# Optimization experiments

Measured on AMD Instinct MI355X. Metric: run time of the kernel, lower is better.

The kernel has to match this reference:

```python
import jax, jax.numpy as jnp
import numpy as np

DIM = 1      # homological dimension
CARD = 50    # number of diagram points
H, W = 28, 28
D = 2        # len(Ip.shape)


def _cubical(X, dim=DIM, card=CARD):
    """Pure-numpy cubical persistence (gudhi semantics: lower-dim cells get the
    min of incident top-dimensional cells; finite pairs of dimension `dim`,
    positive persistence, sorted by persistence descending; returns flat
    (i,j) pixel indices of birth/death critical top cells, zero-padded to
    2*D*card int32 values). Mirrors the Cubical numpy_function in the repo."""
    X = np.asarray(X, dtype=np.float64)
    Hh, Ww = X.shape
    A, Bc = 2 * Hh - 1, 2 * Ww - 1
    n = A * Bc
    F = np.empty(n)                 # filtration value per cell
    P = np.empty(n, np.int64)       # flat pixel index of the top cell realizing F
    dms = np.empty(n, np.int64)     # cell dimension

    def cands(a, lim):
        if a % 2 == 1:
            return [(a - 1) // 2]
        return [r for r in (a // 2 - 1, a // 2) if 0 <= r < lim]

    for a in range(A):
        ris = cands(a, Hh)
        for b in range(Bc):
            cjs = cands(b, Ww)
            best = None
            bp = 0
            for r in ris:
                for c in cjs:
                    v = X[r, c]
                    if best is None or v < best:
                        best = v
                        bp = r * Ww + c
            idx = a * Bc + b
            F[idx] = best
            P[idx] = bp
            dms[idx] = (a & 1) + (b & 1)

    order = np.lexsort((np.arange(n), dms, F))   # sort by (F, dim, index)
    pos = np.empty(n, np.int64)
    pos[order] = np.arange(n)

    def faces(cell):
        a, b = divmod(cell, Bc)
        fs = []
        if a & 1:
            fs += [(a - 1) * Bc + b, (a + 1) * Bc + b]
        if b & 1:
            fs += [a * Bc + b - 1, a * Bc + b + 1]
        return fs

    # standard Z/2 boundary-matrix reduction
    Rcols = {}
    low_to_col = {}
    pairs = []
    for j in range(n):
        cell = order[j]
        col = set(int(pos[f]) for f in faces(cell))
        while col:
            l = max(col)
            k = low_to_col.get(l)
            if k is None:
                break
            col ^= Rcols[k]
        if col:
            l = max(col)
            low_to_col[l] = j
            Rcols[j] = col
            pairs.append((l, j))

    rows, pers = [], []
    for (i, j) in pairs:
        bc, dc = order[i], order[j]
        if dms[bc] != dim:
            continue
        pr = F[dc] - F[bc]
        if pr <= 0:
            continue
        rows.append((int(P[bc]), int(P[dc])))
        pers.append(pr)
    if rows:
        srt = np.argsort(np.asarray(pers))[::-1]   # persistence descending
        rows = [rows[k] for k in srt]

    inds = []
    for k in range(min(card, len(rows))):
        bi, di = rows[k]
        inds += [bi // Ww, bi % Ww, di // Ww, di % Ww]
    inds += [0] * (2 * D * card - len(inds))
    return np.asarray(inds, dtype=np.int32)


def setup_inputs() -> dict:
    key = jax.random.key(0)
    k1, k2 = jax.random.split(key)
    I = jax.random.normal(k1, (H, W, 2), dtype=jnp.float32)
    p = jax.random.normal(k2, (2, 1), dtype=jnp.float32)
    return {"I": I, "p": p}


def reference(I, p):
    # Ip = reshape(tensordot(I, p, 1), [28, 28])
    Ip = jnp.reshape(jnp.tensordot(I, p, 1), (H, W))
    inds = jax.pure_callback(
        lambda x: _cubical(np.asarray(x)),
        jax.ShapeDtypeStruct((2 * D * CARD,), jnp.int32),
        Ip,
    )
    inds = jax.lax.stop_gradient(inds).reshape(-1, D)   # [2*card, 2]
    # gather_nd(Ip, inds) then reshape to [card, 2]
    dgm = Ip[inds[:, 0], inds[:, 1]].reshape(-1, 2)
    return dgm
```

## Files before the change

### kernel.cpp

```cpp
#include <hip/hip_runtime.h>

#define IMG_H 28
#define IMG_W 28
#define AA 55
#define NCELL 3025
#define NEDGE 1512
#define NSQ 729
#define CARD 50
#define NW 24
#define CAP 160
#define BS 1024

typedef unsigned long long u64;
typedef unsigned int u32;
typedef unsigned short u16;

#define OFF_KEYSE   0
#define OFF_KEYSS   16384
#define OFF_IP      24576
#define OFF_RANKE   27712
#define OFF_RANKSQ  30736
#define OFF_COL     0
#define OFF_OWNB    30720
#define OFF_CANDA   0
#define OFF_CANDB   8192
#define OFF_BND     43008
#define OFF_EDGEF   48840
#define OFF_SQF     54888
#define OFF_CURLOW  58448
#define OFF_PAIRLOW 60832
#define OFF_NONAPP  62296
#define OFF_SCAL    63768
#define SMEM_TOTAL  63776

__device__ __forceinline__ int edgeCid(int a, int b) {
    return (a & 1) ? (((a - 1) >> 1) * 28 + (b >> 1))
                   : (756 + (a >> 1) * 27 + ((b - 1) >> 1));
}

__device__ __forceinline__ u32 sortable(float f) {
    u32 fb = __float_as_uint(f);
    return (fb & 0x80000000u) ? ~fb : (fb | 0x80000000u);
}
__device__ __forceinline__ float unsortable(u32 v) {
    return __uint_as_float((v & 0x80000000u) ? (v & 0x7FFFFFFFu) : ~v);
}

__device__ __forceinline__ u64 shflx64(u64 v, int s) {
    u32 lo = __shfl_xor((u32)v, s, 64);
    u32 hi = __shfl_xor((u32)(v >> 32), s, 64);
    return ((u64)hi << 32) | lo;
}

__device__ __forceinline__ void cswapDir(u64& a, u64& b, bool up) {
    u64 mn = a < b ? a : b, mx = a < b ? b : a;
    a = up ? mn : mx; b = up ? mx : mn;
}

__device__ __forceinline__ u64 bstage(u64 v, int i, int s, int size) {
    u64 p = shflx64(v, s);
    bool keepmin = (((i & size) == 0) == ((i & s) == 0));
    return keepmin ? (v < p ? v : p) : (v > p ? v : p);
}

__device__ __forceinline__ void sessA(u64& r0, u64& r1, int i0) {
    for (int size = 2; size <= 64; size <<= 1)
        for (int s = size >> 1; s; s >>= 1) {
            r0 = bstage(r0, i0, s, size);
            r1 = bstage(r1, i0 + 64, s, size);
        }
}
__device__ __forceinline__ void sessB(u64& r0, u64& r1, int i0, int size) {
    bool asc = ((i0 & size) == 0);
    { u64 mn = r0 < r1 ? r0 : r1, mx = r0 < r1 ? r1 : r0;
      r0 = asc ? mn : mx; r1 = asc ? mx : mn; }
    for (int s = 32; s; s >>= 1) {
        bool keep = (asc == ((i0 & s) == 0));
        u64 p0 = shflx64(r0, s);
        r0 = keep ? (r0 < p0 ? r0 : p0) : (r0 > p0 ? r0 : p0);
        u64 p1 = shflx64(r1, s);
        r1 = keep ? (r1 < p1 ? r1 : p1) : (r1 > p1 ? r1 : p1);
    }
}

template<int G>
__device__ __forceinline__ void fusedClassicArr(u64* arr, int nElem) {
    const int nG = nElem / G;
    for (int gid = (int)threadIdx.x; gid < nG; gid += BS) {
        int high = gid >> 7, low = gid & 127;
        bool up = ((high & 1) == 0);
        int base = high * G * 128 + low;
        u64 k[G];
        #pragma unroll
        for (int g = 0; g < G; ++g) k[g] = arr[base + g * 128];
        #pragma unroll
        for (int d = G / 2; d >= 1; d >>= 1)
            #pragma unroll
            for (int g = 0; g < G; ++g)
                if (!(g & d)) cswapDir(k[g], k[g | d], up);
        #pragma unroll
        for (int g = 0; g < G; ++g) arr[base + g * 128] = k[g];
    }
}

__device__ __forceinline__ void sessWin(u64* kE, u64* kS, int i0, int size, bool hasS) {
    u64 a = kE[i0], b = kE[i0 + 64];
    sessB(a, b, i0, size);
    kE[i0] = a; kE[i0 + 64] = b;
    if (hasS) {
        u64 c = kS[i0], d = kS[i0 + 64];
        sessB(c, d, i0, size);
        kS[i0] = c; kS[i0 + 64] = d;
    }
}

__device__ __forceinline__ u64 lstage(u64 v, int lane, int s, bool up) {
    u64 p = shflx64(v, s);
    bool keepmin = (up == ((lane & s) == 0));
    return keepmin ? (v < p ? v : p) : (v > p ? v : p);
}

__device__ __forceinline__ u64 sort64(u64 v, int lane) {
    for (int size = 2; size <= 32; size <<= 1)
        for (int s = size >> 1; s; s >>= 1)
            v = lstage(v, lane, s, (lane & size) == 0);
    for (int s = 32; s; s >>= 1)
        v = lstage(v, lane, s, true);
    return v;
}
__device__ __forceinline__ u64 merge64(u64 a, u64 b, int lane) {
    u64 br = shflx64(b, 63);
    u64 m = a < br ? a : br;
    for (int s = 32; s; s >>= 1)
        m = lstage(m, lane, s, true);
    return m;
}

__device__ __forceinline__ void xorOwner(u64 o, u64& w, int lane, const u64* col) {
    if (!(o >> 63)) {
        #pragma unroll
        for (int q = 0; q < 4; ++q) {
            int rr = (int)((o >> (12 * q)) & 0xFFFull);
            if ((rr >> 6) == lane) w ^= 1ull << (rr & 63);
        }
    } else {
        int s = (int)(o & 0xFFFFull);
        if (lane < NW) w ^= col[s * NW + lane];
    }
}

__device__ __forceinline__ int findLow(u64 w, int lane) {
    u64 mask = __ballot(w != 0ull);
    if (mask == 0ull) return 0xFFFE;
    int L = 63 - __builtin_clzll(mask);
    int cand = (lane << 6) + 63 - __builtin_clzll(w | 1ull);
    return __builtin_amdgcn_readlane(cand, L);
}

__global__ __launch_bounds__(BS) void cubical_kernel(const float* __restrict__ I,
                                                     const float* __restrict__ p,
                                                     float* __restrict__ out) {
    __shared__ __align__(16) char smem[SMEM_TOTAL];
    u64*    keysE   = (u64*)(smem + OFF_KEYSE);
    u64*    keysS   = (u64*)(smem + OFF_KEYSS);
    float*  Ip      = (float*)(smem + OFF_IP);
    u16*    rankE   = (u16*)(smem + OFF_RANKE);
    u16*    rankSq  = (u16*)(smem + OFF_RANKSQ);
    u64*    col     = (u64*)(smem + OFF_COL);
    u64*    ownerBnd= (u64*)(smem + OFF_OWNB);
    u64*    candA   = (u64*)(smem + OFF_CANDA);
    u64*    candB   = (u64*)(smem + OFF_CANDB);
    u64*    bnd     = (u64*)(smem + OFF_BND);
    float*  edgeFr  = (float*)(smem + OFF_EDGEF);
    float*  sqF     = (float*)(smem + OFF_SQF);
    u16*    curLow  = (u16*)(smem + OFF_CURLOW);
    u16*    pairLow = (u16*)(smem + OFF_PAIRLOW);
    u16*    nonapp  = (u16*)(smem + OFF_NONAPP);
    float*  padvP   = (float*)(smem + OFF_SCAL);
    int*    Mp      = (int*)(smem + OFF_SCAL + 4);

    const int tid = threadIdx.x;
    const int wave = tid >> 6, lane = tid & 63;

    const float p0 = p[0], p1 = p[1];
    for (int i = tid; i < IMG_H * IMG_W; i += BS) {
        float v = I[2 * i] * p0 + I[2 * i + 1] * p1;
        Ip[i] = v;
        if (i == 0) *padvP = v;
    }
    for (int i = 1512 + tid; i < 2048; i += BS) keysE[i] = ~0ull;
    for (int i = 729 + tid; i < 1024; i += BS) keysS[i] = ~0ull;
    __syncthreads();

    for (int idx = tid; idx < NCELL; idx += BS) {
        int a = idx / AA, b = idx % AA;
        int da = a & 1, db = b & 1;
        int dim = da + db;
        if (dim == 0) continue;
        int r0, r1, c0, c1;
        if (da) { r0 = r1 = (a - 1) >> 1; }
        else    { r1 = a >> 1; r0 = (a == 0) ? r1 : r1 - 1; }
        if (db) { c0 = c1 = (b - 1) >> 1; }
        else    { c1 = b >> 1; c0 = (b == 0) ? c1 : c1 - 1; }
        float best = Ip[r0 * IMG_W + c0];
        best = fminf(best, Ip[r0 * IMG_W + c1]);
        best = fminf(best, Ip[r1 * IMG_W + c0]);
        best = fminf(best, Ip[r1 * IMG_W + c1]);
        u64 key = ((u64)sortable(best) << 12) | (u32)idx;
        if (dim == 1) keysE[edgeCid(a, b)] = key;
        else          keysS[((a - 1) >> 1) * 27 + ((b - 1) >> 1)] = key;
    }
    __syncthreads();

    {
        const int eB = wave * 128 + lane;
        const bool hasS = (wave < 8);
        {
            u64 a = keysE[eB], b = keysE[eB + 64];
            sessA(a, b, eB);
            sessB(a, b, eB, 128);
            keysE[eB] = a; keysE[eB + 64] = b;
            if (hasS) {
                u64 c = keysS[eB], d = keysS[eB + 64];
                sessA(c, d, eB);
                sessB(c, d, eB, 128);
                keysS[eB] = c; keysS[eB + 64] = d;
            }
        }
        __syncthreads();
        fusedClassicArr<2>(keysE, 2048);
        fusedClassicArr<2>(keysS, 1024);
        __syncthreads();
        sessWin(keysE, keysS, eB, 256, hasS);
        __syncthreads();
        fusedClassicArr<4>(keysE, 2048);
        fusedClassicArr<4>(keysS, 1024);
        __syncthreads();
        sessWin(keysE, keysS, eB, 512, hasS);
        __syncthreads();
        fusedClassicArr<8>(keysE, 2048);
        fusedClassicArr<8>(keysS, 1024);
        __syncthreads();
        sessWin(keysE, keysS, eB, 1024, hasS);
        __syncthreads();
        fusedClassicArr<16>(keysE, 2048);
        __syncthreads();
        sessWin(keysE, keysS, eB, 2048, false);
        __syncthreads();
    }

    for (int r = tid; r < NEDGE; r += BS) {
        u64 k = keysE[r];
        int idx = (int)(k & 0xFFFull);
        int a = idx / AA, b = idx % AA;
        rankE[edgeCid(a, b)] = (u16)r;
        edgeFr[r] = unsortable((u32)(k >> 12));
    }
    for (int r = tid; r < NSQ; r += BS) {
        u64 k = keysS[r];
        int idx = (int)(k & 0xFFFull);
        int a = idx / AA, b = idx % AA;
        rankSq[((a - 1) >> 1) * 27 + ((b - 1) >> 1)] = (u16)r;
        sqF[r] = unsortable((u32)(k >> 12));
    }
    __syncthreads();

    for (int j = tid; j < NSQ; j += BS) {
        int sidx = (int)(keysS[j] & 0xFFFull);
        int a = sidx / AA, b = sidx % AA;
        int ec[4] = { sidx - AA, sidx + AA, sidx - 1, sidx + 1 };
        int er[4];
        er[0] = rankE[edgeCid(a - 1, b)];
        er[1] = rankE[edgeCid(a + 1, b)];
        er[2] = rankE[edgeCid(a, b - 1)];
        er[3] = rankE[edgeCid(a, b + 1)];
        bnd[j] = (u64)er[0] | ((u64)er[1] << 16) | ((u64)er[2] << 32) | ((u64)er[3] << 48);
        int bq = 0;
        if (er[1] > er[bq]) bq = 1;
        if (er[2] > er[bq]) bq = 2;
        if (er[3] > er[bq]) bq = 3;
        int ecell = ec[bq];
        int x = ecell / AA, y = ecell % AA;
        u32 rmin = 0xFFFFFFFFu;
        if (x & 1) {
            if (y >= 2)  rmin = rankSq[((x - 1) >> 1) * 27 + ((y - 2) >> 1)];
            if (y <= 52) { u32 r2 = rankSq[((x - 1) >> 1) * 27 + (y >> 1)]; rmin = min(rmin, r2); }
        } else {
            if (x >= 2)  rmin = rankSq[((x - 2) >> 1) * 27 + ((y - 1) >> 1)];
            if (x <= 52) { u32 r2 = rankSq[(x >> 1) * 27 + ((y - 1) >> 1)]; rmin = min(rmin, r2); }
        }
        pairLow[j] = (rmin == (u32)j) ? (u16)(0x8000u | er[bq]) : (u16)0xFFFFu;
    }
    __syncthreads();

    for (int i = tid; i < 1536; i += BS) ownerBnd[i] = ~0ull;
    __syncthreads();
    for (int j = tid; j < NSQ; j += BS) {
        u16 pl = pairLow[j];
        if (pl != 0xFFFFu) {
            u64 bd = bnd[j];
            u64 e = (bd & 0xFFFull) | (((bd >> 16) & 0xFFFull) << 12)
                  | (((bd >> 32) & 0xFFFull) << 24) | (((bd >> 48) & 0xFFFull) << 36);
            ownerBnd[pl & 0x7FFF] = e;
        }
    }
    if (tid < 64) {
        int cnt = 0;
        for (int base = 0; base < NSQ; base += 64) {
            int j = base + lane;
            bool f = (j < NSQ) && (pairLow[j] == 0xFFFFu);
            u64 m = __ballot(f);
            int pfx = __popcll(m & ((1ull << lane) - 1ull));
            if (f) nonapp[cnt + pfx] = (u16)j;
            cnt += __popcll(m);
        }
        if (lane == 0) *Mp = (cnt > CAP) ? CAP : cnt;
    }
    __syncthreads();
    const int M = *Mp;

    for (int idx = tid; idx < M * NW; idx += BS) {
        int slot = idx / NW, w = idx - slot * NW;
        u64 bd = bnd[nonapp[slot]];
        u64 x = 0ull;
        #pragma unroll
        for (int q = 0; q < 4; ++q) {
            int rr = (int)((bd >> (16 * q)) & 0xFFFFull);
            if ((rr >> 6) == w) x ^= 1ull << (rr & 63);
        }
        col[idx] = x;
    }
    if (tid < M) {
        u64 bd = bnd[nonapp[tid]];
        int mx = 0;
        #pragma unroll
        for (int q = 0; q < 4; ++q) {
            int rr = (int)((bd >> (16 * q)) & 0xFFFFull);
            if (rr > mx) mx = rr;
        }
        curLow[tid] = (u16)mx;
    }
    __syncthreads();

    {
        const int nWaves = BS / 64;
        for (int li = wave; li < M; li += nWaves) {
            int slot = li;
            u64 myEnc = (1ull << 63) | (u64)slot;
            u64 w = (lane < NW) ? col[slot * NW + lane] : 0ull;
            int low = (int)curLow[slot];
            for (;;) {
                if (low == 0xFFFE) {
                    if (lane == 0) curLow[slot] = (u16)0xFFFE;
                    break;
                }
                u64 o = *(volatile u64*)&ownerBnd[low];
                if (o < myEnc) {
                    xorOwner(o, w, lane, col);
                    low = findLow(w, lane);
                    continue;
                }
                if (lane < NW) col[slot * NW + lane] = w;
                __threadfence_block();
                u64 got = 0;
                if (lane == 0) {
                    u64 cur = *(volatile u64*)&ownerBnd[low];
                    while (myEnc < cur) {
                        u64 prev = atomicCAS(&ownerBnd[low], cur, myEnc);
                        if (prev == cur) break;
                        cur = prev;
                    }
                    got = cur;
                }
                u32 glo = __builtin_amdgcn_readlane((u32)got, 0);
                u32 ghi = __builtin_amdgcn_readlane((u32)(got >> 32), 0);
                got = ((u64)ghi << 32) | glo;
                if (got < myEnc) {
                    xorOwner(got, w, lane, col);
                    low = findLow(w, lane);
                    continue;
                }
                if (lane == 0) curLow[slot] = (u16)low;
                if (got == ~0ull) break;
                __threadfence_block();
                slot = (int)(got & 0xFFFFull);
                myEnc = got;
                w = (lane < NW) ? col[slot * NW + lane] : 0ull;
            }
        }
        __syncthreads();
    }
    if (tid < M) {
        u16 cl = curLow[tid];
        pairLow[nonapp[tid]] = (cl == 0xFFFEu) ? (u16)0xFFFDu : cl;
    }
    __syncthreads();

    {
        if (wave < 12) {
            int i = wave * 64 + lane;
            u64 key = ~0ull;
            if (i < NSQ) {
                int pl = (int)pairLow[i];
                if (pl != 0xFFFD && pl != 0xFFFF) {
                    int low = pl & 0x7FFF;
                    double pr = (double)sqF[i] - (double)edgeFr[low];
                    if (pr > 0.0) {
                        u64 bits = (u64)__double_as_longlong(pr);
                        key = ~((bits & ~0xFFFull) | (u64)(u32)i);
                    }
                }
            }
            candA[wave * 64 + lane] = sort64(key, lane);
        }
        __syncthreads();
        if (wave < 6) {
            u64 a = candA[(2 * wave) * 64 + lane];
            u64 b = candA[(2 * wave + 1) * 64 + lane];
            candB[wave * 64 + lane] = merge64(a, b, lane);
        }
        __syncthreads();
        if (wave < 3) {
            u64 a = candB[(2 * wave) * 64 + lane];
            u64 b = candB[(2 * wave + 1) * 64 + lane];
            candA[wave * 64 + lane] = merge64(a, b, lane);
        }
        __syncthreads();
        if (wave == 0) {
            u64 a = candA[lane], b = candA[64 + lane], c = candA[128 + lane];
            u64 f = merge64(merge64(a, b, lane), c, lane);
            if (lane < CARD) {
                float bv, dv;
                if (f != ~0ull) {
                    u64 kb = ~f;
                    int j = (int)(kb & 0xFFFull);
                    int low = (int)pairLow[j] & 0x7FFF;
                    bv = edgeFr[low];
                    dv = sqF[j];
                } else {
                    bv = *padvP; dv = *padvP;
                }
                out[2 * lane]     = bv;
                out[2 * lane + 1] = dv;
            }
        }
    }
}

extern "C" void kernel_launch(void* const* d_in, const int* in_sizes, int n_in,
                              void* d_out, int out_size, void* d_ws, size_t ws_size,
                              hipStream_t stream) {
    const float* I = (const float*)d_in[0];
    const float* p = (const float*)d_in[1];
    float* out = (float*)d_out;
    hipLaunchKernelGGL(cubical_kernel, dim3(1), dim3(BS), 0, stream, I, p, out);
}
```

Baseline: 95.16 us.

## Interleave two reduction columns per wave with dynamic work queue and atomicMin claims

Restructures the parallel boundary-matrix reduction so each wave carries two independent columns at once, overlapping their shared-memory loads to hide latency. Work is handed out through an atomic ticket counter instead of a static wave-strided assignment, which balances uneven column reduction lengths. The CAS retry loop for claiming a pivot is replaced by a single atomicMin, and a displaced column is folded into the current working column right away. The cost is higher register pressure and more complex control flow, with possible divergence between the two in-flight columns.

```diff
diff --git a/kernel.cpp b/kernel.cpp
--- a/kernel.cpp
+++ b/kernel.cpp
@@ -31,7 +31,7 @@
 #define OFF_PAIRLOW 60832
 #define OFF_NONAPP  62296
 #define OFF_SCAL    63768
-#define SMEM_TOTAL  63776
+#define SMEM_TOTAL  63784
 
 __device__ __forceinline__ int edgeCid(int a, int b) {
     return (a & 1) ? (((a - 1) >> 1) * 28 + (b >> 1))
@@ -136,16 +136,11 @@
     return m;
 }
 
-__device__ __forceinline__ void xorOwner(u64 o, u64& w, int lane, const u64* col) {
-    if (!(o >> 63)) {
-        #pragma unroll
-        for (int q = 0; q < 4; ++q) {
-            int rr = (int)((o >> (12 * q)) & 0xFFFull);
-            if ((rr >> 6) == lane) w ^= 1ull << (rr & 63);
-        }
-    } else {
-        int s = (int)(o & 0xFFFFull);
-        if (lane < NW) w ^= col[s * NW + lane];
+__device__ __forceinline__ void xorInline(u64 o, u64& w, int lane) {
+    #pragma unroll
+    for (int q = 0; q < 4; ++q) {
+        int rr = (int)((o >> (12 * q)) & 0xFFFull);
+        if ((rr >> 6) == lane) w ^= 1ull << (rr & 63);
     }
 }
 
@@ -155,6 +150,12 @@
     int L = 63 - __builtin_clzll(mask);
     int cand = (lane << 6) + 63 - __builtin_clzll(w | 1ull);
     return __builtin_amdgcn_readlane(cand, L);
+}
+
+__device__ __forceinline__ u64 bcast64lane0(u64 v) {
+    u32 lo = __builtin_amdgcn_readfirstlane((u32)v);
+    u32 hi = __builtin_amdgcn_readfirstlane((u32)(v >> 32));
+    return ((u64)hi << 32) | lo;
 }
 
 __global__ __launch_bounds__(BS) void cubical_kernel(const float* __restrict__ I,
@@ -178,6 +179,7 @@
     u16*    nonapp  = (u16*)(smem + OFF_NONAPP);
     float*  padvP   = (float*)(smem + OFF_SCAL);
     int*    Mp      = (int*)(smem + OFF_SCAL + 4);
+    int*    tickP   = (int*)(smem + OFF_SCAL + 8);
 
     const int tid = threadIdx.x;
     const int wave = tid >> 6, lane = tid & 63;
@@ -340,52 +342,101 @@
         }
         curLow[tid] = (u16)mx;
     }
+    if (tid == 0) *tickP = 0;
     __syncthreads();
 
     {
-        const int nWaves = BS / 64;
-        for (int li = wave; li < M; li += nWaves) {
-            int slot = li;
-            u64 myEnc = (1ull << 63) | (u64)slot;
-            u64 w = (lane < NW) ? col[slot * NW + lane] : 0ull;
-            int low = (int)curLow[slot];
-            for (;;) {
+        int  slotA = 0, lowA = 0;  u64 encA = 0, wA = 0;  bool actA = false;
+        int  slotB = 0, lowB = 0;  u64 encB = 0, wB = 0;  bool actB = false;
+
+        auto refill = [&](int& slot, int& low, u64& enc, u64& w, bool& act) {
+            u32 t = 0;
+            if (lane == 0) t = (u32)atomicAdd(tickP, 1);
+            t = __builtin_amdgcn_readfirstlane(t);
+            if ((int)t < M) {
+                slot = (int)t;
+                enc = (1ull << 63) | (u64)t;
+                w = (lane < NW) ? *(volatile u64*)&col[(int)t * NW + lane] : 0ull;
+                low = (int)curLow[t];
+                act = true;
+            } else {
+                act = false;
+            }
+        };
+
+        auto claim = [&](int& slot, int& low, u64& enc, u64& w, bool& act) {
+            if (lane < NW) *(volatile u64*)&col[slot * NW + lane] = w;
+            __threadfence_block();
+            u64 old = 0;
+            if (lane == 0)
+                old = (u64)atomicMin((unsigned long long*)&ownerBnd[low],
+                                     (unsigned long long)enc);
+            old = bcast64lane0(old);
+            if (old < enc) {
+                if (old >> 63) {
+                    int vs = (int)(old & 0xFFFFull);
+                    if (lane < NW) w ^= *(volatile u64*)&col[vs * NW + lane];
+                } else {
+                    xorInline(old, w, lane);
+                }
+                low = findLow(w, lane);
                 if (low == 0xFFFE) {
                     if (lane == 0) curLow[slot] = (u16)0xFFFE;
-                    break;
-                }
-                u64 o = *(volatile u64*)&ownerBnd[low];
-                if (o < myEnc) {
-                    xorOwner(o, w, lane, col);
+                    refill(slot, low, enc, w, act);
+                }
+            } else {
+                if (lane == 0) curLow[slot] = (u16)low;
+                if (old == ~0ull) {
+                    refill(slot, low, enc, w, act);
+                } else {
+                    int vs = (int)(old & 0xFFFFull);
+                    u64 cv = (lane < NW) ? *(volatile u64*)&col[vs * NW + lane] : 0ull;
+                    w = cv ^ w;
+                    slot = vs; enc = old;
                     low = findLow(w, lane);
-                    continue;
-                }
-                if (lane < NW) col[slot * NW + lane] = w;
-                __threadfence_block();
-                u64 got = 0;
-                if (lane == 0) {
-                    u64 cur = *(volatile u64*)&ownerBnd[low];
-                    while (myEnc < cur) {
-                        u64 prev = atomicCAS(&ownerBnd[low], cur, myEnc);
-                        if (prev == cur) break;
-                        cur = prev;
+                    if (low == 0xFFFE) {
+                        if (lane == 0) curLow[slot] = (u16)0xFFFE;
+                        refill(slot, low, enc, w, act);
                     }
-                    got = cur;
-                }
-                u32 glo = __builtin_amdgcn_readlane((u32)got, 0);
-                u32 ghi = __builtin_amdgcn_readlane((u32)(got >> 32), 0);
-                got = ((u64)ghi << 32) | glo;
-                if (got < myEnc) {
-                    xorOwner(got, w, lane, col);
-                    low = findLow(w, lane);
-                    continue;
-                }
-                if (lane == 0) curLow[slot] = (u16)low;
-                if (got == ~0ull) break;
-                __threadfence_block();
-                slot = (int)(got & 0xFFFFull);
-                myEnc = got;
-                w = (lane < NW) ? col[slot * NW + lane] : 0ull;
+                }
+            }
+        };
+
+        refill(slotA, lowA, encA, wA, actA);
+        refill(slotB, lowB, encB, wB, actB);
+
+        while (actA || actB) {
+            u64 oA = 0, oB = 0;
+            if (actA) oA = *(volatile u64*)&ownerBnd[lowA];
+            if (actB) oB = *(volatile u64*)&ownerBnd[lowB];
+            bool xA = actA && (oA < encA);
+            bool xB = actB && (oB < encB);
+            bool sA = xA && (oA >> 63);
+            bool sB = xB && (oB >> 63);
+            u64 cA = 0, cB = 0;
+            if (sA && lane < NW)
+                cA = *(volatile u64*)&col[(int)(oA & 0xFFFFull) * NW + lane];
+            if (sB && lane < NW)
+                cB = *(volatile u64*)&col[(int)(oB & 0xFFFFull) * NW + lane];
+            if (xA) {
+                if (sA) wA ^= cA; else xorInline(oA, wA, lane);
+                lowA = findLow(wA, lane);
+                if (lowA == 0xFFFE) {
+                    if (lane == 0) curLow[slotA] = (u16)0xFFFE;
+                    refill(slotA, lowA, encA, wA, actA);
+                }
+            } else if (actA) {
+                claim(slotA, lowA, encA, wA, actA);
+            }
+            if (xB) {
+                if (sB) wB ^= cB; else xorInline(oB, wB, lane);
+                lowB = findLow(wB, lane);
+                if (lowB == 0xFFFE) {
+                    if (lane == 0) curLow[slotB] = (u16)0xFFFE;
+                    refill(slotB, lowB, encB, wB, actB);
+                }
+            } else if (actB) {
+                claim(slotB, lowB, encB, wB, actB);
             }
         }
         __syncthreads();
```

After: 104.9 us. +10.2%, slower.

## Split waves into half-wave column reducers with dynamic ticket work queue

Applied to the files above, without the earlier changes.

The parallel boundary-matrix reduction now runs two columns per wavefront, one per 32-lane half, instead of one column per wave with a static stride. Columns are handed out dynamically through a shared atomic ticket counter. The CAS loop is replaced by a single atomicMin, and the per-iteration branches are flattened into predicated, ballot-guarded steps. This aims to double the number of concurrent reducers and cut load imbalance and serial round trips. The cost is lanes idling when the two halves diverge, plus more complex lock-free logic that could hide correctness races.

```diff
diff --git a/kernel.cpp b/kernel.cpp
--- a/kernel.cpp
+++ b/kernel.cpp
@@ -31,7 +31,7 @@
 #define OFF_PAIRLOW 60832
 #define OFF_NONAPP  62296
 #define OFF_SCAL    63768
-#define SMEM_TOTAL  63776
+#define SMEM_TOTAL  63784
 
 __device__ __forceinline__ int edgeCid(int a, int b) {
     return (a & 1) ? (((a - 1) >> 1) * 28 + (b >> 1))
@@ -44,6 +44,13 @@
 }
 __device__ __forceinline__ float unsortable(u32 v) {
     return __uint_as_float((v & 0x80000000u) ? (v & 0x7FFFFFFFu) : ~v);
+}
+
+__device__ __forceinline__ u64 ldrelax(u64* p) {
+    return __hip_atomic_load(p, __ATOMIC_RELAXED, __HIP_MEMORY_SCOPE_WORKGROUP);
+}
+__device__ __forceinline__ void strelax(u64* p, u64 v) {
+    __hip_atomic_store(p, v, __ATOMIC_RELAXED, __HIP_MEMORY_SCOPE_WORKGROUP);
 }
 
 __device__ __forceinline__ u64 shflx64(u64 v, int s) {
@@ -136,25 +143,20 @@
     return m;
 }
 
-__device__ __forceinline__ void xorOwner(u64 o, u64& w, int lane, const u64* col) {
-    if (!(o >> 63)) {
-        #pragma unroll
-        for (int q = 0; q < 4; ++q) {
-            int rr = (int)((o >> (12 * q)) & 0xFFFull);
-            if ((rr >> 6) == lane) w ^= 1ull << (rr & 63);
-        }
-    } else {
-        int s = (int)(o & 0xFFFFull);
-        if (lane < NW) w ^= col[s * NW + lane];
-    }
-}
-
-__device__ __forceinline__ int findLow(u64 w, int lane) {
-    u64 mask = __ballot(w != 0ull);
-    if (mask == 0ull) return 0xFFFE;
-    int L = 63 - __builtin_clzll(mask);
-    int cand = (lane << 6) + 63 - __builtin_clzll(w | 1ull);
-    return __builtin_amdgcn_readlane(cand, L);
+__device__ __forceinline__ u64 appXorMask(u64 o, int sub) {
+    u64 x = 0ull;
+    #pragma unroll
+    for (int q = 0; q < 4; ++q) {
+        int rr = (int)((o >> (12 * q)) & 0xFFFull);
+        x ^= ((rr >> 6) == sub) ? (1ull << (rr & 63)) : 0ull;
+    }
+    return x;
+}
+
+__device__ __forceinline__ u64 bcastlane64(u64 v, int l) {
+    u32 lo = (u32)__builtin_amdgcn_readlane((int)(u32)v, l);
+    u32 hi = (u32)__builtin_amdgcn_readlane((int)(u32)(v >> 32), l);
+    return ((u64)hi << 32) | lo;
 }
 
 __global__ __launch_bounds__(BS) void cubical_kernel(const float* __restrict__ I,
@@ -178,6 +180,7 @@
     u16*    nonapp  = (u16*)(smem + OFF_NONAPP);
     float*  padvP   = (float*)(smem + OFF_SCAL);
     int*    Mp      = (int*)(smem + OFF_SCAL + 4);
+    int*    tickP   = (int*)(smem + OFF_SCAL + 8);
 
     const int tid = threadIdx.x;
     const int wave = tid >> 6, lane = tid & 63;
@@ -340,52 +343,99 @@
         }
         curLow[tid] = (u16)mx;
     }
+    if (tid == 0) *tickP = 32;
     __syncthreads();
 
     {
-        const int nWaves = BS / 64;
-        for (int li = wave; li < M; li += nWaves) {
-            int slot = li;
-            u64 myEnc = (1ull << 63) | (u64)slot;
-            u64 w = (lane < NW) ? col[slot * NW + lane] : 0ull;
-            int low = (int)curLow[slot];
-            for (;;) {
-                if (low == 0xFFFE) {
-                    if (lane == 0) curLow[slot] = (u16)0xFFFE;
-                    break;
+        const int sub   = lane & 31;
+        const int halfB = lane >> 5;
+        int  slot = wave * 2 + halfB;
+        bool act  = (slot < M);
+        u64  enc  = (1ull << 63) | (u64)slot;
+        u64  w    = 0ull;
+        int  low  = 0;
+        if (act) {
+            if (sub < NW) w = ldrelax(&col[slot * NW + sub]);
+            low = (int)curLow[slot];
+        }
+
+        while (__ballot(act) != 0ull) {
+            int oAddr = act ? low : 0;
+            u64 o = ldrelax(&ownerBnd[oAddr]);
+            bool doXor   = act && (o < enc);
+            bool settled = doXor && (o >> 63);
+            u64 cx = 0ull;
+            if (__ballot(settled) != 0ull) {
+                int csub = (sub < NW) ? sub : 0;
+                int vsl  = settled ? (int)(o & 0xFFFFull) : 0;
+                u64 c = ldrelax(&col[vsl * NW + csub]);
+                cx = (settled && sub < NW) ? c : 0ull;
+            }
+            bool doClaim = act && !doXor;
+            u64 old = 0ull;
+            if (__ballot(doClaim) != 0ull) {
+                if (doClaim && sub < NW) strelax(&col[slot * NW + sub], w);
+                __threadfence_block();
+                u64 oldv = 0ull;
+                if (doClaim && sub == 0)
+                    oldv = (u64)atomicMin((unsigned long long*)&ownerBnd[low],
+                                          (unsigned long long)enc);
+                u64 oA = bcastlane64(oldv, 0);
+                u64 oB = bcastlane64(oldv, 32);
+                old = halfB ? oB : oA;
+            }
+            bool lost  = doClaim && (old < enc);
+            bool lostS = lost && (old >> 63);
+            bool rested  = doClaim && !lost;
+            if (rested && sub == 0) curLow[slot] = (u16)low;
+            bool inherit = rested && (old != ~0ull);
+            u64 c2x = 0ull;
+            if (__ballot(lostS || inherit) != 0ull) {
+                bool rd = (lostS || inherit);
+                int csub = (sub < NW) ? sub : 0;
+                int vsl  = rd ? (int)(old & 0xFFFFull) : 0;
+                u64 c2 = ldrelax(&col[vsl * NW + csub]);
+                c2x = (rd && sub < NW) ? c2 : 0ull;
+            }
+            u64 ax  = appXorMask(o, sub);
+            u64 ax2 = appXorMask(old, sub);
+            w ^= (settled ? cx : 0ull)
+               ^ ((doXor && !settled) ? ax : 0ull)
+               ^ ((lostS || inherit) ? c2x : 0ull)
+               ^ ((lost && !lostS) ? ax2 : 0ull);
+            if (inherit) { slot = (int)(old & 0xFFFFull); enc = old; }
+            bool restedEmpty = rested && (old == ~0ull);
+            bool changed = doXor || lost || inherit;
+            u64 mask = __ballot(w != 0ull);
+            u32 mA = (u32)mask, mB = (u32)(mask >> 32);
+            int cand = (sub << 6) + 63 - __builtin_clzll(w | 1ull);
+            int LA = 31 - __builtin_clz(mA | 1u);
+            int LB = 31 - __builtin_clz(mB | 1u);
+            int cA = __builtin_amdgcn_readlane(cand, LA);
+            int cB = __builtin_amdgcn_readlane(cand, 32 + LB);
+            int nlA = mA ? cA : 0xFFFE;
+            int nlB = mB ? cB : 0xFFFE;
+            int nl = halfB ? nlB : nlA;
+            if (changed) low = nl;
+            bool died = changed && (nl == 0xFFFE);
+            if (died && sub == 0) curLow[slot] = (u16)0xFFFE;
+            bool refillNeed = died || restedEmpty;
+            if (__ballot(refillNeed) != 0ull) {
+                u32 t = 0;
+                if (refillNeed && sub == 0) t = (u32)atomicAdd(tickP, 1);
+                u32 tA = (u32)__builtin_amdgcn_readlane((int)t, 0);
+                u32 tB = (u32)__builtin_amdgcn_readlane((int)t, 32);
+                u32 myt = halfB ? tB : tA;
+                if (refillNeed) {
+                    if ((int)myt < M) {
+                        slot = (int)myt;
+                        enc  = (1ull << 63) | (u64)myt;
+                        w    = (sub < NW) ? ldrelax(&col[(int)myt * NW + sub]) : 0ull;
+                        low  = (int)curLow[myt];
+                    } else {
+                        act = false; w = 0ull;
+                    }
                 }
-                u64 o = *(volatile u64*)&ownerBnd[low];
-                if (o < myEnc) {
-                    xorOwner(o, w, lane, col);
-                    low = findLow(w, lane);
-                    continue;
-                }
-                if (lane < NW) col[slot * NW + lane] = w;
-                __threadfence_block();
-                u64 got = 0;
-                if (lane == 0) {
-                    u64 cur = *(volatile u64*)&ownerBnd[low];
-                    while (myEnc < cur) {
-                        u64 prev = atomicCAS(&ownerBnd[low], cur, myEnc);
-                        if (prev == cur) break;
-                        cur = prev;
-                    }
-                    got = cur;
-                }
-                u32 glo = __builtin_amdgcn_readlane((u32)got, 0);
-                u32 ghi = __builtin_amdgcn_readlane((u32)(got >> 32), 0);
-                got = ((u64)ghi << 32) | glo;
-                if (got < myEnc) {
-                    xorOwner(got, w, lane, col);
-                    low = findLow(w, lane);
-                    continue;
-                }
-                if (lane == 0) curLow[slot] = (u16)low;
-                if (got == ~0ull) break;
-                __threadfence_block();
-                slot = (int)(got & 0xFFFFull);
-                myEnc = got;
-                w = (lane < NW) ? col[slot * NW + lane] : 0ull;
             }
         }
         __syncthreads();
```

Result: slower. 104.8 us (+10.1%).
